# Performance work log

Measured on AMD Instinct MI355X. Metric: run time of the kernel, lower is better.

The kernel has to match this reference:

```python
import jax, jax.numpy as jnp
import numpy as np

N, IN_CHN, MDIM, ATT_D, NUM_CLS = 100000, 1024, 512, 128, 2
NUM_GROUP, INST_PER_GROUP = 8, 4
GROUP_SIZE = N // NUM_GROUP


def setup_inputs() -> dict:
    key = jax.random.key(0)
    ks = jax.random.split(key, 8)
    def w(k, shape, fan):
        return (jax.random.normal(k, shape, jnp.float32) / np.sqrt(fan)).astype(jnp.float32)
    return {
        "index_chunk_list": jax.random.randint(ks[0], (NUM_GROUP, GROUP_SIZE), 0, N),
        "tfeat_tensor": jax.random.normal(ks[1], (N, IN_CHN), jnp.float32),
        # DimReduction: Linear(1024 -> mDim) + ReLU (numLayer_Res = 0)
        "W1": w(ks[2], (MDIM, IN_CHN), IN_CHN), "b1": jnp.zeros((MDIM,), jnp.float32),
        # Attention: Linear(mDim -> 128), tanh, Linear(128 -> 1)
        "Wa1": w(ks[3], (ATT_D, MDIM), MDIM), "ba1": jnp.zeros((ATT_D,), jnp.float32),
        "Wa2": w(ks[4], (1, ATT_D), ATT_D), "ba2": jnp.zeros((1,), jnp.float32),
        # Classifier_1fc: Linear(mDim -> num_cls)  (dropout=0 -> identity)
        "Wc": w(ks[5], (NUM_CLS, MDIM), MDIM), "bc": jnp.zeros((NUM_CLS,), jnp.float32),
    }


def _group_forward(idx, tfeat, W1, b1, Wa1, ba1, Wa2, ba2, Wc, bc):
    # idx: [S] instance indices for one pseudo-bag
    sub = jnp.take(tfeat, idx, axis=0)                       # [S, in_chn]  gather
    mid = jax.nn.relu(sub @ W1.T + b1)                       # [S, m]       DimReduction
    a = jnp.tanh(mid @ Wa1.T + ba1) @ Wa2.T + ba2            # [S, 1]       Attention logits
    a = jax.nn.softmax(a[:, 0], axis=0)                      # [S]          softmax over instances
    att = mid * a[:, None]                                   # [S, m]       einsum('ns,n->ns')
    bag = att.sum(axis=0)                                    # [m]          attention-weighted sum
    pred = bag @ Wc.T + bc                                    # [C]          bag-level logits
    # get_cam_1d: per-instance logits from classifier weight only (no bias)
    cam = jax.nn.softmax(att @ Wc.T, axis=1)                  # [S, C]
    order = jnp.argsort(-cam[:, -1])                          # descending sort on last-class prob
    topk = jnp.concatenate([order[:INST_PER_GROUP], order[-INST_PER_GROUP:]])
    maxmin = jnp.take(mid, topk, axis=0)                      # [2k, m]  MaxMinS distill feats
    return pred, maxmin


def reference(index_chunk_list, tfeat_tensor, W1, b1, Wa1, ba1, Wa2, ba2, Wc, bc):
    f = jax.vmap(_group_forward, in_axes=(0,) + (None,) * 9)
    slide_sub_preds, slide_pseudo_feat = f(index_chunk_list, tfeat_tensor,
                                           W1, b1, Wa1, ba1, Wa2, ba2, Wc, bc)
    # [numGroup, num_cls], [numGroup, 2*instance_per_group, mDim]
    return slide_sub_preds, slide_pseudo_feat
```

## Files before the change

### kernel.cpp

```cpp
#include <hip/hip_runtime.h>
#include <stdint.h>

#define N_TOT 100000
#define IN_CHN 1024
#define MDIM 512
#define ATT_D 128
#define NUM_GROUP 8
#define GROUP_SIZE 12500
#define SEGR 98

typedef __bf16 bf16x8 __attribute__((ext_vector_type(8)));
typedef float f32x4 __attribute__((ext_vector_type(4)));
typedef unsigned short u16x8 __attribute__((ext_vector_type(8)));

__device__ __forceinline__ unsigned short f2bf(float x){
  union { float f; unsigned u; } v; v.f = x;
  unsigned r = v.u + 0x7fffu + ((v.u >> 16) & 1u);
  return (unsigned short)(r >> 16);
}
__device__ __forceinline__ float bf2f(unsigned short h){
  union { unsigned u; float f; } v; v.u = ((unsigned)h) << 16; return v.f;
}
__device__ __forceinline__ void gload16(const void* g, void* l){
  __builtin_amdgcn_global_load_lds(
      (const __attribute__((address_space(1))) unsigned int*)g,
      (__attribute__((address_space(3))) unsigned int*)l, 16, 0, 0);
}

__global__ __launch_bounds__(256) void kconv(const float* __restrict__ W1,
                                             const float* __restrict__ Wa1,
                                             unsigned short* __restrict__ W1b,
                                             unsigned short* __restrict__ Wa1b){
  int i = blockIdx.x * 256 + threadIdx.x;
  if (i < MDIM * IN_CHN) W1b[i] = f2bf(W1[i]);
  else {
    int j = i - MDIM * IN_CHN;
    if (j < ATT_D * MDIM) Wa1b[j] = f2bf(Wa1[j]);
  }
}

__global__ __launch_bounds__(512) void kgemm_mid(const int* __restrict__ idxf,
                                                 const float* __restrict__ tfeat,
                                                 const unsigned short* __restrict__ W1b,
                                                 const float* __restrict__ b1,
                                                 unsigned short* __restrict__ midb){
  __shared__ alignas(16) float Af[128 * 32];
  __shared__ alignas(16) unsigned short Bs[256 * 32];
  __shared__ int gsm[128];
  int tid = threadIdx.x;
  int xcd = blockIdx.x & 7, idx = blockIdx.x >> 3;
  int tile = (xcd < 4 ? xcd * 196 : 4 * 196 + (xcd - 4) * 195) + idx;
  int bn = tile & 1, bm = tile >> 1;
  int m0 = bm * 128, n0 = bn * 256;
  if (tid < 128){ int r = m0 + tid; gsm[tid] = idxf[r < N_TOT ? r : 0]; }
  __syncthreads();

  int w = tid >> 6, l = tid & 63;
  int l16 = tid & 15, hi = (tid >> 4) & 3;
  int wm = w >> 2, wn = w & 3;

  const float* asrc[2]; int adst[2];
  #pragma unroll
  for (int q = 0; q < 2; q++){
    int rowl = q * 64 + w * 8 + (l >> 3);
    asrc[q] = tfeat + (size_t)gsm[rowl] * IN_CHN + (((l & 7) ^ (l >> 3)) << 2);
    adst[q] = (q * 64 + w * 8) * 32;
  }
  const unsigned short* bsrc[2]; int bdst[2];
  #pragma unroll
  for (int q = 0; q < 2; q++){
    int rowl = q * 128 + w * 16 + (l >> 2);
    bsrc[q] = W1b + (size_t)(n0 + rowl) * IN_CHN + (((l & 3) ^ ((l >> 3) & 3)) << 3);
    bdst[q] = (q * 128 + w * 16) * 32;
  }

  f32x4 acc[4][4];
  #pragma unroll
  for (int a = 0; a < 4; a++)
    #pragma unroll
    for (int b = 0; b < 4; b++) acc[a][b] = (f32x4){0.f, 0.f, 0.f, 0.f};

  int r7 = l16 & 7;
  int b3 = (l16 >> 1) & 3;

  for (int s = 0; s < 32; s++){
    __syncthreads();
    #pragma unroll
    for (int q = 0; q < 2; q++){
      gload16(asrc[q] + s * 32, &Af[adst[q]]);
      gload16(bsrc[q] + s * 32, &Bs[bdst[q]]);
    }
    __syncthreads();

    bf16x8 af[4], bfr[4];
    #pragma unroll
    for (int a = 0; a < 4; a++){
      int row = wm * 64 + a * 16 + l16;
      f32x4 lo  = *(const f32x4*)&Af[row * 32 + (((2 * hi) ^ r7) << 2)];
      f32x4 hi4 = *(const f32x4*)&Af[row * 32 + (((2 * hi + 1) ^ r7) << 2)];
      bf16x8 pk;
      pk[0] = (__bf16)lo[0]; pk[1] = (__bf16)lo[1]; pk[2] = (__bf16)lo[2]; pk[3] = (__bf16)lo[3];
      pk[4] = (__bf16)hi4[0]; pk[5] = (__bf16)hi4[1]; pk[6] = (__bf16)hi4[2]; pk[7] = (__bf16)hi4[3];
      af[a] = pk;
    }
    #pragma unroll
    for (int b = 0; b < 4; b++){
      int row = wn * 64 + b * 16 + l16;
      bfr[b] = *(const bf16x8*)&Bs[row * 32 + ((hi ^ b3) << 3)];
    }
    #pragma unroll
    for (int a = 0; a < 4; a++)
      #pragma unroll
      for (int b = 0; b < 4; b++)
        acc[a][b] = __builtin_amdgcn_mfma_f32_16x16x32_bf16(af[a], bfr[b], acc[a][b], 0, 0, 0);
  }

  #pragma unroll
  for (int b = 0; b < 4; b++){
    int col = n0 + wn * 64 + b * 16 + l16;
    float bias = b1[col];
    #pragma unroll
    for (int a = 0; a < 4; a++){
      int rbase = m0 + wm * 64 + a * 16 + hi * 4;
      #pragma unroll
      for (int q = 0; q < 4; q++){
        int row = rbase + q;
        if (row < N_TOT){
          float v = acc[a][b][q] + bias;
          midb[(size_t)row * MDIM + col] = f2bf(fmaxf(v, 0.f));
        }
      }
    }
  }
}

__global__ __launch_bounds__(256) void kattn(const unsigned short* __restrict__ midb,
                                             const unsigned short* __restrict__ Wa1b,
                                             const float* __restrict__ ba1,
                                             const float* __restrict__ Wa2,
                                             const float* __restrict__ ba2,
                                             const float* __restrict__ Wc,
                                             float* __restrict__ lv,
                                             float* __restrict__ tv){
  __shared__ alignas(16) unsigned short Asm[128 * 64];
  __shared__ alignas(16) unsigned short Bsm[128 * 64];
  __shared__ float dsh[512];
  __shared__ float part[128][2];
  int tid = threadIdx.x;
  int m0 = blockIdx.x * 128;
  for (int i = tid; i < 512; i += 256) dsh[i] = Wc[512 + i] - Wc[i];

  int w = tid >> 6, l = tid & 63;
  int l16 = tid & 15, hi = (tid >> 4) & 3;
  int wm = tid >> 7, wn = (tid >> 6) & 1;
  int scw = (l & 7) ^ (l >> 3);

  const unsigned short *asrc[4], *bsrc[4];
  int dsto[4];
  #pragma unroll
  for (int q = 0; q < 4; q++){
    int rowl = q * 32 + w * 8 + (l >> 3);
    asrc[q] = midb + (size_t)(m0 + rowl) * MDIM + scw * 8;
    bsrc[q] = Wa1b + (size_t)rowl * MDIM + scw * 8;
    dsto[q] = (q * 32 + w * 8) * 64;
  }

  f32x4 acc[4][4];
  #pragma unroll
  for (int a = 0; a < 4; a++)
    #pragma unroll
    for (int b = 0; b < 4; b++) acc[a][b] = (f32x4){0.f, 0.f, 0.f, 0.f};
  int r7 = l16 & 7;

  int rt = tid >> 1, kh = tid & 1;
  int rt7 = rt & 7;
  float t = 0.f;

  for (int s = 0; s < 8; s++){
    __syncthreads();
    #pragma unroll
    for (int q = 0; q < 4; q++){
      gload16(asrc[q] + s * 64, &Asm[dsto[q]]);
      gload16(bsrc[q] + s * 64, &Bsm[dsto[q]]);
    }
    __syncthreads();
    #pragma unroll
    for (int ks = 0; ks < 2; ks++){
      bf16x8 af[4], bfr[4];
      #pragma unroll
      for (int a = 0; a < 4; a++){
        int row = wm * 64 + a * 16 + l16;
        af[a] = *(const bf16x8*)&Asm[row * 64 + (((ks * 4 + hi) ^ r7) << 3)];
      }
      #pragma unroll
      for (int b = 0; b < 4; b++){
        int row = wn * 64 + b * 16 + l16;
        bfr[b] = *(const bf16x8*)&Bsm[row * 64 + (((ks * 4 + hi) ^ r7) << 3)];
      }
      #pragma unroll
      for (int a = 0; a < 4; a++)
        #pragma unroll
        for (int b = 0; b < 4; b++)
          acc[a][b] = __builtin_amdgcn_mfma_f32_16x16x32_bf16(af[a], bfr[b], acc[a][b], 0, 0, 0);
    }
    #pragma unroll
    for (int j = 0; j < 4; j++){
      int gc = kh * 4 + j;
      u16x8 v = *(const u16x8*)&Asm[rt * 64 + ((gc ^ rt7) << 3)];
      int kb = s * 64 + gc * 8;
      #pragma unroll
      for (int e = 0; e < 8; e++) t += bf2f((unsigned short)v[e]) * dsh[kb + e];
    }
  }
  t += __shfl_xor(t, 1);
  if (kh == 0){
    int row = m0 + rt;
    if (row < N_TOT) tv[row] = t;
  }
  #pragma unroll
  for (int a = 0; a < 4; a++){
    #pragma unroll
    for (int q = 0; q < 4; q++){
      float v = 0.f;
      #pragma unroll
      for (int b = 0; b < 4; b++){
        int col = wn * 64 + b * 16 + l16;
        v += tanhf(acc[a][b][q] + ba1[col]) * Wa2[col];
      }
      #pragma unroll
      for (int off = 1; off < 16; off <<= 1) v += __shfl_xor(v, off);
      if (l16 == 0) part[wm * 64 + a * 16 + hi * 4 + q][wn] = v;
    }
  }
  __syncthreads();
  if (tid < 128){
    int row = m0 + tid;
    if (row < N_TOT) lv[row] = part[tid][0] + part[tid][1] + ba2[0];
  }
}

__global__ __launch_bounds__(256) void kselect(const float* __restrict__ lv,
                                               const float* __restrict__ tv,
                                               float* __restrict__ maxlw, float* __restrict__ Zw,
                                               int* __restrict__ cand,
                                               float* __restrict__ w){
  __shared__ float keys[GROUP_SIZE];
  __shared__ float candk[4096];
  __shared__ int   candi[4096];
  __shared__ float rk[256];
  __shared__ int ri[256];
  __shared__ int rs[256];
  __shared__ float sbc;
  int g = blockIdx.x, tid = threadIdx.x;
  const float* lg = lv + (size_t)g * GROUP_SIZE;
  const float* tg = tv + (size_t)g * GROUP_SIZE;

  float mx = -1e30f;
  for (int i = tid; i < GROUP_SIZE; i += 256) mx = fmaxf(mx, lg[i]);
  rk[tid] = mx; __syncthreads();
  for (int s = 128; s > 0; s >>= 1){ if (tid < s) rk[tid] = fmaxf(rk[tid], rk[tid + s]); __syncthreads(); }
  if (tid == 0) sbc = rk[0];
  __syncthreads();
  float maxl = sbc;

  float z = 0.f;
  for (int i = tid; i < GROUP_SIZE; i += 256){
    float ez = expf(lg[i] - maxl);
    z += ez;
    keys[i] = ez * tg[i];
  }
  rk[tid] = z; __syncthreads();
  for (int s = 128; s > 0; s >>= 1){ if (tid < s) rk[tid] += rk[tid + s]; __syncthreads(); }
  if (tid == 0){ maxlw[g] = maxl; Zw[g] = rk[0]; }
  __syncthreads();
  float invZ = 1.0f / rk[0];
  for (int i = tid; i < GROUP_SIZE; i += 256)
    w[(size_t)g * GROUP_SIZE + i] = expf(lg[i] - maxl) * invZ;
  __syncthreads();

  {
    float tk[16]; int tix[16];
    #pragma unroll
    for (int j = 0; j < 16; j++){ tk[j] = -1e30f; tix[j] = 0x7fffffff; }
    for (int i = tid; i < GROUP_SIZE; i += 256){
      float ck = keys[i];
      if (ck > tk[15]){
        int ci = i;
        #pragma unroll
        for (int j = 0; j < 16; j++){
          bool ins = ck > tk[j];
          float nk = ins ? ck : tk[j]; int ni = ins ? ci : tix[j];
          float ok = ins ? tk[j] : ck; int oi = ins ? tix[j] : ci;
          tk[j] = nk; tix[j] = ni; ck = ok; ci = oi;
        }
      }
    }
    #pragma unroll
    for (int j = 0; j < 16; j++){ candk[tid * 16 + j] = tk[j]; candi[tid * 16 + j] = tix[j]; }
  }
  __syncthreads();
  for (int it = 0; it < 16; it++){
    float bk = -1e30f; int bi = 0x7fffffff; int bs = -1;
    for (int jj = tid; jj < 4096; jj += 256){
      float k = candk[jj]; int ix = candi[jj];
      if (k > bk || (k == bk && ix < bi)){ bk = k; bi = ix; bs = jj; }
    }
    rk[tid] = bk; ri[tid] = bi; rs[tid] = bs; __syncthreads();
    for (int s = 128; s > 0; s >>= 1){
      if (tid < s){
        if (rk[tid + s] > rk[tid] || (rk[tid + s] == rk[tid] && ri[tid + s] < ri[tid])){
          rk[tid] = rk[tid + s]; ri[tid] = ri[tid + s]; rs[tid] = rs[tid + s];
        }
      }
      __syncthreads();
    }
    if (tid == 0){ cand[g * 32 + it] = ri[0]; candk[rs[0]] = -1e30f; }
    __syncthreads();
  }

  {
    float tk[16]; int tix[16];
    #pragma unroll
    for (int j = 0; j < 16; j++){ tk[j] = 1e30f; tix[j] = -1; }
    for (int i = tid; i < GROUP_SIZE; i += 256){
      float ck = keys[i];
      if (ck <= tk[15]){
        int ci = i;
        #pragma unroll
        for (int j = 0; j < 16; j++){
          bool ins = ck <= tk[j];
          float nk = ins ? ck : tk[j]; int ni = ins ? ci : tix[j];
          float ok = ins ? tk[j] : ck; int oi = ins ? tix[j] : ci;
          tk[j] = nk; tix[j] = ni; ck = ok; ci = oi;
        }
      }
    }
    #pragma unroll
    for (int j = 0; j < 16; j++){ candk[tid * 16 + j] = tk[j]; candi[tid * 16 + j] = tix[j]; }
  }
  __syncthreads();
  for (int it = 0; it < 16; it++){
    float bk = 1e30f; int bi = -1; int bs = -1;
    for (int jj = tid; jj < 4096; jj += 256){
      float k = candk[jj]; int ix = candi[jj];
      if (k < bk || (k == bk && ix > bi)){ bk = k; bi = ix; bs = jj; }
    }
    rk[tid] = bk; ri[tid] = bi; rs[tid] = bs; __syncthreads();
    for (int s = 128; s > 0; s >>= 1){
      if (tid < s){
        if (rk[tid + s] < rk[tid] || (rk[tid + s] == rk[tid] && ri[tid + s] > ri[tid])){
          rk[tid] = rk[tid + s]; ri[tid] = ri[tid + s]; rs[tid] = rs[tid + s];
        }
      }
      __syncthreads();
    }
    if (tid == 0){ cand[g * 32 + 16 + it] = ri[0]; candk[rs[0]] = 1e30f; }
    __syncthreads();
  }
}

__global__ __launch_bounds__(256) void kexact(const int* __restrict__ idxf,
                                              const float* __restrict__ tfeat,
                                              const float* __restrict__ W1,
                                              const float* __restrict__ b1,
                                              const float* __restrict__ Wa1,
                                              const float* __restrict__ ba1,
                                              const float* __restrict__ Wa2,
                                              const float* __restrict__ ba2,
                                              const float* __restrict__ Wc,
                                              const int* __restrict__ cand,
                                              const float* __restrict__ maxlw,
                                              float* __restrict__ emid, float* __restrict__ ekey){
  __shared__ float subs[1024];
  __shared__ float midc[512];
  __shared__ float hs[128];
  __shared__ float red[256];
  __shared__ float tsh;
  int bid = blockIdx.x; int g = bid >> 5, c = bid & 31; int tid = threadIdx.x;
  int s = cand[g * 32 + c];
  int inst = idxf[g * GROUP_SIZE + s];
  ((float4*)subs)[tid] = ((const float4*)(tfeat + (size_t)inst * IN_CHN))[tid];
  __syncthreads();

  float a0 = b1[tid], a1 = b1[tid + 256];
  const float4* w0 = (const float4*)(W1 + (size_t)tid * IN_CHN);
  const float4* w1 = (const float4*)(W1 + ((size_t)tid + 256) * IN_CHN);
  const float4* s4 = (const float4*)subs;
  #pragma unroll 4
  for (int k = 0; k < 256; k++){
    float4 sv = s4[k], wva = w0[k], wvb = w1[k];
    a0 += sv.x * wva.x + sv.y * wva.y + sv.z * wva.z + sv.w * wva.w;
    a1 += sv.x * wvb.x + sv.y * wvb.y + sv.z * wvb.z + sv.w * wvb.w;
  }
  a0 = fmaxf(a0, 0.f); a1 = fmaxf(a1, 0.f);
  midc[tid] = a0; midc[tid + 256] = a1;
  size_t eo = (size_t)(g * 32 + c) * MDIM;
  emid[eo + tid] = a0; emid[eo + tid + 256] = a1;
  __syncthreads();

  if (tid < 128){
    const float4* wr = (const float4*)(Wa1 + (size_t)tid * MDIM);
    const float4* m4 = (const float4*)midc;
    float h = ba1[tid];
    #pragma unroll 4
    for (int j = 0; j < 128; j++){
      float4 mv = m4[j], wv = wr[j];
      h += mv.x * wv.x + mv.y * wv.y + mv.z * wv.z + mv.w * wv.w;
    }
    hs[tid] = tanhf(h) * Wa2[tid];
  }
  __syncthreads();

  float tp = midc[tid] * (Wc[512 + tid] - Wc[tid]) + midc[tid + 256] * (Wc[768 + tid] - Wc[256 + tid]);
  red[tid] = tp; __syncthreads();
  for (int st = 128; st > 0; st >>= 1){ if (tid < st) red[tid] += red[tid + st]; __syncthreads(); }
  if (tid == 0) tsh = red[0];
  __syncthreads();
  red[tid] = (tid < 128) ? hs[tid] : 0.f; __syncthreads();
  for (int st = 128; st > 0; st >>= 1){ if (tid < st) red[tid] += red[tid + st]; __syncthreads(); }
  if (tid == 0){
    float lval = red[0] + ba2[0];
    ekey[g * 32 + c] = expf(lval - maxlw[g]) * tsh;
  }
}

__global__ __launch_bounds__(256) void kbag(const unsigned short* __restrict__ midb,
                                            const float* __restrict__ w,
                                            float* __restrict__ bagp){
  __shared__ float wl[SEGR];
  int g = blockIdx.x >> 7, seg = blockIdx.x & 127, tid = threadIdx.x;
  int i0 = seg * SEGR;
  int nr = GROUP_SIZE - i0; if (nr > SEGR) nr = SEGR;
  size_t base = (size_t)g * GROUP_SIZE;
  if (tid < nr) wl[tid] = w[base + i0 + tid];
  __syncthreads();
  float a0 = 0.f, a1 = 0.f;
  const unsigned short* mp = midb + (base + i0) * MDIM + 2 * tid;
  int i = 0;
  for (; i + 2 <= nr; i += 2){
    unsigned pk0 = *(const unsigned*)(mp + (size_t)i * MDIM);
    unsigned pk1 = *(const unsigned*)(mp + (size_t)(i + 1) * MDIM);
    float w0 = wl[i], w1 = wl[i + 1];
    a0 += w0 * bf2f((unsigned short)(pk0 & 0xffff)) + w1 * bf2f((unsigned short)(pk1 & 0xffff));
    a1 += w0 * bf2f((unsigned short)(pk0 >> 16)) + w1 * bf2f((unsigned short)(pk1 >> 16));
  }
  if (i < nr){
    unsigned pk0 = *(const unsigned*)(mp + (size_t)i * MDIM);
    float w0 = wl[i];
    a0 += w0 * bf2f((unsigned short)(pk0 & 0xffff));
    a1 += w0 * bf2f((unsigned short)(pk0 >> 16));
  }
  float* dst = bagp + (size_t)blockIdx.x * MDIM + 2 * tid;
  dst[0] = a0; dst[1] = a1;
}

__global__ __launch_bounds__(256) void kfinal(const float* __restrict__ bagp,
                                              const float* __restrict__ Wc,
                                              const float* __restrict__ bc,
                                              const float* __restrict__ emid,
                                              const float* __restrict__ ekey,
                                              const int* __restrict__ cand,
                                              float* __restrict__ out){
  __shared__ float k32[32];
  __shared__ int s32[32];
  __shared__ int ordv[32];
  __shared__ float r0[256], r1[256];
  int g = blockIdx.x, tid = threadIdx.x;
  if (tid < 32){ k32[tid] = ekey[g * 32 + tid]; s32[tid] = cand[g * 32 + tid]; }
  __syncthreads();
  if (tid == 0){
    unsigned used = 0;
    for (int a = 0; a < 32; a++){
      int best = -1;
      for (int b = 0; b < 32; b++){
        if ((used >> b) & 1u) continue;
        if (best < 0 || k32[b] > k32[best] || (k32[b] == k32[best] && s32[b] < s32[best])) best = b;
      }
      used |= 1u << best;
      ordv[a] = best;
    }
  }
  float p0 = 0.f, p1 = 0.f;
  for (int j = tid; j < 512; j += 256){
    float bv = 0.f;
    for (int s2 = 0; s2 < 128; s2++) bv += bagp[(size_t)(g * 128 + s2) * MDIM + j];
    p0 += bv * Wc[j];
    p1 += bv * Wc[512 + j];
  }
  r0[tid] = p0; r1[tid] = p1; __syncthreads();
  for (int s = 128; s > 0; s >>= 1){ if (tid < s){ r0[tid] += r0[tid + s]; r1[tid] += r1[tid + s]; } __syncthreads(); }
  if (tid == 0){
    out[g * 2 + 0] = r0[0] + bc[0];
    out[g * 2 + 1] = r1[0] + bc[1];
  }
  __syncthreads();
  for (int p = 0; p < 8; p++){
    int cc = ordv[p < 4 ? p : 24 + p];
    const float* src = emid + (size_t)(g * 32 + cc) * MDIM;
    float* dst = out + 16 + (size_t)(g * 8 + p) * MDIM;
    for (int j = tid; j < 512; j += 256) dst[j] = src[j];
  }
}

extern "C" void kernel_launch(void* const* d_in, const int* in_sizes, int n_in,
                              void* d_out, int out_size, void* d_ws, size_t ws_size,
                              hipStream_t stream){
  const int*   idxf = (const int*)d_in[0];
  const float* tfeat= (const float*)d_in[1];
  const float* W1   = (const float*)d_in[2];
  const float* b1   = (const float*)d_in[3];
  const float* Wa1  = (const float*)d_in[4];
  const float* ba1  = (const float*)d_in[5];
  const float* Wa2  = (const float*)d_in[6];
  const float* ba2  = (const float*)d_in[7];
  const float* Wc   = (const float*)d_in[8];
  const float* bc   = (const float*)d_in[9];
  float* out = (float*)d_out;
  (void)in_sizes; (void)n_in; (void)out_size; (void)ws_size;

  char* ws = (char*)d_ws;
  size_t off = 0;
  auto alloc = [&](size_t bytes){ void* p = ws + off; off += (bytes + 255) & ~(size_t)255; return p; };
  float* lv    = (float*)alloc((size_t)N_TOT * 4);
  float* tv    = (float*)alloc((size_t)N_TOT * 4);
  float* maxlw = (float*)alloc(NUM_GROUP * 4);
  float* Zw    = (float*)alloc(NUM_GROUP * 4);
  int*   cand  = (int*)alloc(NUM_GROUP * 32 * 4);
  float* ekey  = (float*)alloc(NUM_GROUP * 32 * 4);
  float* emid  = (float*)alloc((size_t)NUM_GROUP * 32 * MDIM * 4);
  float* bagp  = (float*)alloc((size_t)NUM_GROUP * 128 * MDIM * 4);
  unsigned short* W1b  = (unsigned short*)alloc((size_t)MDIM * IN_CHN * 2);
  unsigned short* Wa1b = (unsigned short*)alloc((size_t)ATT_D * MDIM * 2);
  unsigned short* midb = (unsigned short*)alloc((size_t)N_TOT * MDIM * 2);
  float* w = tv;

  kconv<<<2304, 256, 0, stream>>>(W1, Wa1, W1b, Wa1b);
  kgemm_mid<<<1564, 512, 0, stream>>>(idxf, tfeat, W1b, b1, midb);
  kattn<<<782, 256, 0, stream>>>(midb, Wa1b, ba1, Wa2, ba2, Wc, lv, tv);
  kselect<<<8, 256, 0, stream>>>(lv, tv, maxlw, Zw, cand, w);
  kexact<<<256, 256, 0, stream>>>(idxf, tfeat, W1, b1, Wa1, ba1, Wa2, ba2, Wc, cand, maxlw, emid, ekey);
  kbag<<<1024, 256, 0, stream>>>(midb, w, bagp);
  kfinal<<<8, 256, 0, stream>>>(bagp, Wc, bc, emid, ekey, cand, out);
}
```

Before: 647.0 us.

## Fuse class-difference dot into GEMM epilogue and vectorize bag reduction

The per-instance projection onto Wc[1]-Wc[0] now happens in the mid GEMM epilogue. Each N-half tile writes fp32 partials that kselect sums, so kattn no longer rescans mid from LDS for that dot. The projection now uses the fp32 activations rather than their bf16-rounded copies. kbag is rewritten to use 16-byte bf16 loads with four row-groups reduced through LDS and 64 segments per group instead of 128, and kfinal is adjusted to match. The epilogue gains shuffle reductions, an extra barrier and more LDS.

```diff
diff --git a/kernel.cpp b/kernel.cpp
--- a/kernel.cpp
+++ b/kernel.cpp
@@ -7,7 +7,7 @@
 #define ATT_D 128
 #define NUM_GROUP 8
 #define GROUP_SIZE 12500
-#define SEGR 98
+#define SEGB 196
 
 typedef __bf16 bf16x8 __attribute__((ext_vector_type(8)));
 typedef float f32x4 __attribute__((ext_vector_type(4)));
@@ -43,16 +43,24 @@
                                                  const float* __restrict__ tfeat,
                                                  const unsigned short* __restrict__ W1b,
                                                  const float* __restrict__ b1,
-                                                 unsigned short* __restrict__ midb){
+                                                 const float* __restrict__ Wc,
+                                                 unsigned short* __restrict__ midb,
+                                                 float* __restrict__ tvp){
   __shared__ alignas(16) float Af[128 * 32];
   __shared__ alignas(16) unsigned short Bs[256 * 32];
   __shared__ int gsm[128];
+  __shared__ float dcol[256];
+  __shared__ float tvacc[128][4];
   int tid = threadIdx.x;
   int xcd = blockIdx.x & 7, idx = blockIdx.x >> 3;
   int tile = (xcd < 4 ? xcd * 196 : 4 * 196 + (xcd - 4) * 195) + idx;
   int bn = tile & 1, bm = tile >> 1;
   int m0 = bm * 128, n0 = bn * 256;
   if (tid < 128){ int r = m0 + tid; gsm[tid] = idxf[r < N_TOT ? r : 0]; }
+  if (tid >= 128 && tid < 384){
+    int c = tid - 128;
+    dcol[c] = Wc[512 + n0 + c] - Wc[n0 + c];
+  }
   __syncthreads();
 
   int w = tid >> 6, l = tid & 63;
@@ -115,22 +123,32 @@
         acc[a][b] = __builtin_amdgcn_mfma_f32_16x16x32_bf16(af[a], bfr[b], acc[a][b], 0, 0, 0);
   }
 
-  #pragma unroll
-  for (int b = 0; b < 4; b++){
-    int col = n0 + wn * 64 + b * 16 + l16;
-    float bias = b1[col];
-    #pragma unroll
-    for (int a = 0; a < 4; a++){
-      int rbase = m0 + wm * 64 + a * 16 + hi * 4;
-      #pragma unroll
-      for (int q = 0; q < 4; q++){
-        int row = rbase + q;
-        if (row < N_TOT){
-          float v = acc[a][b][q] + bias;
-          midb[(size_t)row * MDIM + col] = f2bf(fmaxf(v, 0.f));
-        }
-      }
-    }
+  float biasv[4];
+  #pragma unroll
+  for (int b = 0; b < 4; b++) biasv[b] = b1[n0 + wn * 64 + b * 16 + l16];
+  #pragma unroll
+  for (int a = 0; a < 4; a++){
+    #pragma unroll
+    for (int q = 0; q < 4; q++){
+      int row = m0 + wm * 64 + a * 16 + hi * 4 + q;
+      float t = 0.f;
+      #pragma unroll
+      for (int b = 0; b < 4; b++){
+        int colL = wn * 64 + b * 16 + l16;
+        float v = fmaxf(acc[a][b][q] + biasv[b], 0.f);
+        t += v * dcol[colL];
+        if (row < N_TOT) midb[(size_t)row * MDIM + n0 + colL] = f2bf(v);
+      }
+      t += __shfl_xor(t, 1); t += __shfl_xor(t, 2);
+      t += __shfl_xor(t, 4); t += __shfl_xor(t, 8);
+      if (l16 == 0) tvacc[wm * 64 + a * 16 + hi * 4 + q][wn] = t;
+    }
+  }
+  __syncthreads();
+  if (tid < 128){
+    int row = m0 + tid;
+    if (row < N_TOT)
+      tvp[(size_t)bn * N_TOT + row] = tvacc[tid][0] + tvacc[tid][1] + tvacc[tid][2] + tvacc[tid][3];
   }
 }
 
@@ -139,16 +157,12 @@
                                              const float* __restrict__ ba1,
                                              const float* __restrict__ Wa2,
                                              const float* __restrict__ ba2,
-                                             const float* __restrict__ Wc,
-                                             float* __restrict__ lv,
-                                             float* __restrict__ tv){
+                                             float* __restrict__ lv){
   __shared__ alignas(16) unsigned short Asm[128 * 64];
   __shared__ alignas(16) unsigned short Bsm[128 * 64];
-  __shared__ float dsh[512];
   __shared__ float part[128][2];
   int tid = threadIdx.x;
   int m0 = blockIdx.x * 128;
-  for (int i = tid; i < 512; i += 256) dsh[i] = Wc[512 + i] - Wc[i];
 
   int w = tid >> 6, l = tid & 63;
   int l16 = tid & 15, hi = (tid >> 4) & 3;
@@ -172,10 +186,6 @@
     for (int b = 0; b < 4; b++) acc[a][b] = (f32x4){0.f, 0.f, 0.f, 0.f};
   int r7 = l16 & 7;
 
-  int rt = tid >> 1, kh = tid & 1;
-  int rt7 = rt & 7;
-  float t = 0.f;
-
   for (int s = 0; s < 8; s++){
     __syncthreads();
     #pragma unroll
@@ -203,19 +213,6 @@
         for (int b = 0; b < 4; b++)
           acc[a][b] = __builtin_amdgcn_mfma_f32_16x16x32_bf16(af[a], bfr[b], acc[a][b], 0, 0, 0);
     }
-    #pragma unroll
-    for (int j = 0; j < 4; j++){
-      int gc = kh * 4 + j;
-      u16x8 v = *(const u16x8*)&Asm[rt * 64 + ((gc ^ rt7) << 3)];
-      int kb = s * 64 + gc * 8;
-      #pragma unroll
-      for (int e = 0; e < 8; e++) t += bf2f((unsigned short)v[e]) * dsh[kb + e];
-    }
-  }
-  t += __shfl_xor(t, 1);
-  if (kh == 0){
-    int row = m0 + rt;
-    if (row < N_TOT) tv[row] = t;
   }
   #pragma unroll
   for (int a = 0; a < 4; a++){
@@ -240,7 +237,7 @@
 }
 
 __global__ __launch_bounds__(256) void kselect(const float* __restrict__ lv,
-                                               const float* __restrict__ tv,
+                                               const float* __restrict__ tvp,
                                                float* __restrict__ maxlw, float* __restrict__ Zw,
                                                int* __restrict__ cand,
                                                float* __restrict__ w){
@@ -253,7 +250,6 @@
   __shared__ float sbc;
   int g = blockIdx.x, tid = threadIdx.x;
   const float* lg = lv + (size_t)g * GROUP_SIZE;
-  const float* tg = tv + (size_t)g * GROUP_SIZE;
 
   float mx = -1e30f;
   for (int i = tid; i < GROUP_SIZE; i += 256) mx = fmaxf(mx, lg[i]);
@@ -267,7 +263,8 @@
   for (int i = tid; i < GROUP_SIZE; i += 256){
     float ez = expf(lg[i] - maxl);
     z += ez;
-    keys[i] = ez * tg[i];
+    size_t gi = (size_t)g * GROUP_SIZE + i;
+    keys[i] = ez * (tvp[gi] + tvp[N_TOT + gi]);
   }
   rk[tid] = z; __syncthreads();
   for (int s = 128; s > 0; s >>= 1){ if (tid < s) rk[tid] += rk[tid + s]; __syncthreads(); }
@@ -427,31 +424,34 @@
 __global__ __launch_bounds__(256) void kbag(const unsigned short* __restrict__ midb,
                                             const float* __restrict__ w,
                                             float* __restrict__ bagp){
-  __shared__ float wl[SEGR];
-  int g = blockIdx.x >> 7, seg = blockIdx.x & 127, tid = threadIdx.x;
-  int i0 = seg * SEGR;
-  int nr = GROUP_SIZE - i0; if (nr > SEGR) nr = SEGR;
+  __shared__ float wl[SEGB];
+  __shared__ float red[4][512];
+  int g = blockIdx.x >> 6, seg = blockIdx.x & 63, tid = threadIdx.x;
+  int rg = tid >> 6, lane = tid & 63;
+  int i0 = seg * SEGB;
+  int nr = GROUP_SIZE - i0; if (nr > SEGB) nr = SEGB;
   size_t base = (size_t)g * GROUP_SIZE;
   if (tid < nr) wl[tid] = w[base + i0 + tid];
   __syncthreads();
-  float a0 = 0.f, a1 = 0.f;
-  const unsigned short* mp = midb + (base + i0) * MDIM + 2 * tid;
-  int i = 0;
-  for (; i + 2 <= nr; i += 2){
-    unsigned pk0 = *(const unsigned*)(mp + (size_t)i * MDIM);
-    unsigned pk1 = *(const unsigned*)(mp + (size_t)(i + 1) * MDIM);
-    float w0 = wl[i], w1 = wl[i + 1];
-    a0 += w0 * bf2f((unsigned short)(pk0 & 0xffff)) + w1 * bf2f((unsigned short)(pk1 & 0xffff));
-    a1 += w0 * bf2f((unsigned short)(pk0 >> 16)) + w1 * bf2f((unsigned short)(pk1 >> 16));
-  }
-  if (i < nr){
-    unsigned pk0 = *(const unsigned*)(mp + (size_t)i * MDIM);
-    float w0 = wl[i];
-    a0 += w0 * bf2f((unsigned short)(pk0 & 0xffff));
-    a1 += w0 * bf2f((unsigned short)(pk0 >> 16));
-  }
-  float* dst = bagp + (size_t)blockIdx.x * MDIM + 2 * tid;
-  dst[0] = a0; dst[1] = a1;
+  float a[8] = {0.f,0.f,0.f,0.f,0.f,0.f,0.f,0.f};
+  const unsigned short* mp = midb + (base + i0) * MDIM + lane * 8;
+  for (int i = rg; i < nr; i += 4){
+    float wi = wl[i];
+    u16x8 v = *(const u16x8*)(mp + (size_t)i * MDIM);
+    #pragma unroll
+    for (int e = 0; e < 8; e++) a[e] += wi * bf2f((unsigned short)v[e]);
+  }
+  #pragma unroll
+  for (int e = 0; e < 8; e++) red[rg][lane * 8 + e] = a[e];
+  __syncthreads();
+  if (rg == 0){
+    float* dst = bagp + (size_t)blockIdx.x * MDIM + lane * 8;
+    #pragma unroll
+    for (int e = 0; e < 8; e++){
+      int c = lane * 8 + e;
+      dst[e] = red[0][c] + red[1][c] + red[2][c] + red[3][c];
+    }
+  }
 }
 
 __global__ __launch_bounds__(256) void kfinal(const float* __restrict__ bagp,
@@ -483,7 +483,7 @@
   float p0 = 0.f, p1 = 0.f;
   for (int j = tid; j < 512; j += 256){
     float bv = 0.f;
-    for (int s2 = 0; s2 < 128; s2++) bv += bagp[(size_t)(g * 128 + s2) * MDIM + j];
+    for (int s2 = 0; s2 < 64; s2++) bv += bagp[(size_t)(g * 64 + s2) * MDIM + j];
     p0 += bv * Wc[j];
     p1 += bv * Wc[512 + j];
   }
@@ -522,23 +522,23 @@
   size_t off = 0;
   auto alloc = [&](size_t bytes){ void* p = ws + off; off += (bytes + 255) & ~(size_t)255; return p; };
   float* lv    = (float*)alloc((size_t)N_TOT * 4);
-  float* tv    = (float*)alloc((size_t)N_TOT * 4);
+  float* tvp   = (float*)alloc((size_t)2 * N_TOT * 4);
   float* maxlw = (float*)alloc(NUM_GROUP * 4);
   float* Zw    = (float*)alloc(NUM_GROUP * 4);
   int*   cand  = (int*)alloc(NUM_GROUP * 32 * 4);
   float* ekey  = (float*)alloc(NUM_GROUP * 32 * 4);
   float* emid  = (float*)alloc((size_t)NUM_GROUP * 32 * MDIM * 4);
-  float* bagp  = (float*)alloc((size_t)NUM_GROUP * 128 * MDIM * 4);
+  float* bagp  = (float*)alloc((size_t)NUM_GROUP * 64 * MDIM * 4);
   unsigned short* W1b  = (unsigned short*)alloc((size_t)MDIM * IN_CHN * 2);
   unsigned short* Wa1b = (unsigned short*)alloc((size_t)ATT_D * MDIM * 2);
   unsigned short* midb = (unsigned short*)alloc((size_t)N_TOT * MDIM * 2);
-  float* w = tv;
+  float* w = tvp;
 
   kconv<<<2304, 256, 0, stream>>>(W1, Wa1, W1b, Wa1b);
-  kgemm_mid<<<1564, 512, 0, stream>>>(idxf, tfeat, W1b, b1, midb);
-  kattn<<<782, 256, 0, stream>>>(midb, Wa1b, ba1, Wa2, ba2, Wc, lv, tv);
-  kselect<<<8, 256, 0, stream>>>(lv, tv, maxlw, Zw, cand, w);
+  kgemm_mid<<<1564, 512, 0, stream>>>(idxf, tfeat, W1b, b1, Wc, midb, tvp);
+  kattn<<<782, 256, 0, stream>>>(midb, Wa1b, ba1, Wa2, ba2, lv);
+  kselect<<<8, 256, 0, stream>>>(lv, tvp, maxlw, Zw, cand, w);
   kexact<<<256, 256, 0, stream>>>(idxf, tfeat, W1, b1, Wa1, ba1, Wa2, ba2, Wc, cand, maxlw, emid, ekey);
-  kbag<<<1024, 256, 0, stream>>>(midb, w, bagp);
+  kbag<<<512, 256, 0, stream>>>(midb, w, bagp);
   kfinal<<<8, 256, 0, stream>>>(bagp, Wc, bc, emid, ekey, cand, out);
 }
```

Result: faster. 622.5 us (-3.8%).
